# Optimization experiments

Measured on AMD Instinct MI355X. Metric: run time of the kernel, lower is better.

Reference implementation:

```python
import jax, jax.numpy as jnp
import numpy as np

B, C, H, W = 16, 32, 32, 2048


def setup_inputs() -> dict:
    key = jax.random.key(0)
    ks = jax.random.split(key, 7)
    s = 1.0 / np.sqrt(C * H)  # torch conv2d default init scale (fan_in = C*H*1)
    x = jax.random.normal(ks[0], (B, C, H, W), dtype=jnp.float32)
    wq = jax.random.uniform(ks[1], (C, C, H), jnp.float32, -s, s)
    bq = jax.random.uniform(ks[2], (C,), jnp.float32, -s, s)
    wk = jax.random.uniform(ks[3], (C, C, H), jnp.float32, -s, s)
    bk = jax.random.uniform(ks[4], (C,), jnp.float32, -s, s)
    wv = jax.random.uniform(ks[5], (C, C, H), jnp.float32, -s, s)
    bv = jax.random.uniform(ks[6], (C,), jnp.float32, -s, s)
    return {"x": x, "wq": wq, "bq": bq, "wk": wk, "bk": bk, "wv": wv, "bv": bv}


def _proj(x, w, b):
    # Conv2d kernel (H,1) with no padding == contract over (in_channels, H).
    # x: [B,C,H,W], w: [Cout,Cin,H] -> [B,Cout,W]
    return jnp.einsum('bihw,oih->bow', x, w) + b[None, :, None]


def reference(x, wq, bq, wk, bk, wv, bv):
    q = _proj(x, wq, bq)            # [B,C,W]
    k = _proj(x, wk, bk)            # [B,C,W]
    v = _proj(x, wv, bv)            # [B,C,W]
    # query.permute(0,2,1) @ key -> [B,W,W]; NOTE: unscaled, as in source.
    scores = jnp.einsum('bcw,bcv->bwv', q, k)
    attn = jax.nn.softmax(scores, axis=-1)
    # value @ attention^T -> [B,C,W]
    out = jnp.einsum('bcv,bwv->bcw', v, attn)
    # bilinear upsample (1,W)->(H,W), align_corners=False: width is identity,
    # height replicates the single row -> pure broadcast. Then residual add.
    return out[:, :, None, :] + x
```

## Files before the change

kernel.cpp:

```cpp
#include <hip/hip_runtime.h>
#include <hip/hip_bf16.h>

typedef __bf16 bf16x8 __attribute__((ext_vector_type(8)));
typedef float  f32x4  __attribute__((ext_vector_type(4)));
typedef float  f32x16 __attribute__((ext_vector_type(16)));

#define NB 16
#define NC 32
#define NH 32
#define NW 2048
#define NK (NC*NH)

static __device__ __forceinline__ unsigned int pk2(float a, float b) {
    union { __bf16 h[2]; unsigned int u; } z;
    z.h[0] = (__bf16)a; z.h[1] = (__bf16)b;
    return z.u;
}

__global__ __launch_bounds__(256) void wprep_kernel(
    const float* __restrict__ wq, const float* __restrict__ wk,
    const float* __restrict__ wv, __bf16* __restrict__ wb)
{
    const int i = blockIdx.x * 256 + threadIdx.x;
    const float* srcs[3] = { wq, wk, wv };
    const float4 v = *(const float4*)(srcs[i >> 13] + (size_t)(i & 8191) * 4);
    union { __bf16 h[4]; unsigned long long u; } z;
    z.h[0] = (__bf16)v.x; z.h[1] = (__bf16)v.y;
    z.h[2] = (__bf16)v.z; z.h[3] = (__bf16)v.w;
    *(unsigned long long*)(wb + (size_t)i * 4) = z.u;
}

__global__ __launch_bounds__(256, 4) void proj_kernel(
    const float* __restrict__ x, const __bf16* __restrict__ wb,
    const float* __restrict__ bq, const float* __restrict__ bk,
    const float* __restrict__ bv,
    __bf16* __restrict__ qT, __bf16* __restrict__ kT, __bf16* __restrict__ V)
{
    const int b    = blockIdx.x >> 6;
    const int wt   = blockIdx.x & 63;
    const int wave = threadIdx.x >> 6;
    const int lane = threadIdx.x & 63;
    const int g    = lane >> 4;
    const int lr   = lane & 15;
    const int w0   = wt * 32;

    const float* xb = x + (size_t)b * NK * NW;
    const int k0 = wave * 256;

    f32x4 acc[2][6];
    #pragma unroll
    for (int mt = 0; mt < 2; ++mt)
        #pragma unroll
        for (int nt = 0; nt < 6; ++nt)
            acc[mt][nt] = f32x4{0.f, 0.f, 0.f, 0.f};

    for (int ki = 0; ki < 8; ++ki) {
        const int kk = k0 + ki * 32;
        bf16x8 af[2];
        #pragma unroll
        for (int mt = 0; mt < 2; ++mt) {
            const float* p = xb + (size_t)(kk + g*8) * NW + (w0 + mt*16 + lr);
            bf16x8 t;
            #pragma unroll
            for (int j = 0; j < 8; ++j) t[j] = (__bf16)p[(size_t)j * NW];
            af[mt] = t;
        }
        bf16x8 bfv[6];
        #pragma unroll
        for (int nt = 0; nt < 6; ++nt)
            bfv[nt] = *(const bf16x8*)(wb + (size_t)(nt >> 1) * 32768
                                          + (size_t)((nt & 1) * 16 + lr) * NK
                                          + kk + g*8);
        #pragma unroll
        for (int mt = 0; mt < 2; ++mt)
            #pragma unroll
            for (int nt = 0; nt < 6; ++nt)
                acc[mt][nt] = __builtin_amdgcn_mfma_f32_16x16x32_bf16(
                    af[mt], bfv[nt], acc[mt][nt], 0, 0, 0);
    }

    __shared__ f32x4 part[4][6][64];
    const float* biases[3] = { bq, bk, bv };
    #pragma unroll
    for (int mt = 0; mt < 2; ++mt) {
        if (mt) __syncthreads();
        #pragma unroll
        for (int nt = 0; nt < 6; ++nt)
            part[wave][nt][lane] = acc[mt][nt];
        __syncthreads();
        #pragma unroll
        for (int q = 0; q < 2; ++q) {
            const int nt = wave + q * 4;
            if (nt < 6) {
                f32x4 s = part[0][nt][lane];
                #pragma unroll
                for (int sl = 1; sl < 4; ++sl) s += part[sl][nt][lane];
                const int pid = nt >> 1;
                const int o   = (nt & 1) * 16 + lr;
                const float bb = biases[pid][o];
                if (pid < 2) {
                    __bf16* dst = (pid ? kT : qT) + (size_t)b * NW * NC;
                    #pragma unroll
                    for (int r = 0; r < 4; ++r) {
                        const int w = w0 + mt*16 + g*4 + r;
                        dst[(size_t)w * NC + o] = (__bf16)(s[r] + bb);
                    }
                } else {
                    union { __bf16 h[4]; unsigned long long u; } z;
                    #pragma unroll
                    for (int r = 0; r < 4; ++r) z.h[r] = (__bf16)(s[r] + bb);
                    __bf16* dst = V + ((size_t)b * NC + o) * NW + (w0 + mt*16 + g*4);
                    *(unsigned long long*)dst = z.u;
                }
            }
        }
    }
}

__global__ __launch_bounds__(512) void attn_kernel(
    const float* __restrict__ x,
    const __bf16* __restrict__ qT, const __bf16* __restrict__ kT,
    const __bf16* __restrict__ V,
    float* __restrict__ out)
{
    const int b    = blockIdx.x >> 6;
    const int wt   = blockIdx.x & 63;
    const int w0   = wt * 32;
    const int wave = threadIdx.x >> 6;
    const int lane = threadIdx.x & 63;
    const int wl = lane & 31, hi = lane >> 5;
    const int swl = (wl & 0x13) | ((wl & 4) << 1) | ((wl & 8) >> 1);

    const __bf16* qTb = qT + (size_t)b * NW * NC;
    const __bf16* kTb = kT + (size_t)b * NW * NC;
    const __bf16* Vb  = V  + (size_t)b * NC * NW;

    const __bf16* qrow = qTb + (size_t)(w0 + wl) * NC;
    const bf16x8 qf0 = *(const bf16x8*)(qrow + hi*8);
    const bf16x8 qf1 = *(const bf16x8*)(qrow + 16 + hi*8);

    f32x16 acc, z16;
    #pragma unroll
    for (int r = 0; r < 16; ++r) { acc[r] = 0.f; z16[r] = 0.f; }
    float m = -1e30f, lsum = 0.f;

    const int vbeg = wave * 256;
    for (int it = 0; it < 8; ++it) {
        const int v0 = vbeg + it * 32;
        const __bf16* krow = kTb + (size_t)(v0 + swl) * NC;
        const bf16x8 kf0 = *(const bf16x8*)(krow + hi*8);
        const bf16x8 kf1 = *(const bf16x8*)(krow + 16 + hi*8);
        const __bf16* vrow = Vb + (size_t)wl * NW + v0;
        const bf16x8 vf0 = *(const bf16x8*)(vrow + hi*8);
        const bf16x8 vf1 = *(const bf16x8*)(vrow + 16 + hi*8);

        f32x16 s = __builtin_amdgcn_mfma_f32_32x32x16_bf16(kf0, qf0, z16, 0, 0, 0);
        s = __builtin_amdgcn_mfma_f32_32x32x16_bf16(kf1, qf1, s, 0, 0, 0);

        float tm[8];
        #pragma unroll
        for (int r = 0; r < 8; ++r) tm[r] = fmaxf(s[r], s[r+8]);
        #pragma unroll
        for (int r = 0; r < 4; ++r) tm[r] = fmaxf(tm[r], tm[r+4]);
        float vm = fmaxf(fmaxf(tm[0], tm[1]), fmaxf(tm[2], tm[3]));
        vm = fmaxf(vm, __shfl_xor(vm, 32));
        const float nm = fmaxf(m, vm);
        const float sc = __expf(m - nm);
        float p[16];
        #pragma unroll
        for (int r = 0; r < 16; ++r) p[r] = __expf(s[r] - nm);
        float ts[8];
        #pragma unroll
        for (int r = 0; r < 8; ++r) ts[r] = p[r] + p[r+8];
        #pragma unroll
        for (int r = 0; r < 4; ++r) ts[r] += ts[r+4];
        float ps = (ts[0] + ts[1]) + (ts[2] + ts[3]);
        ps += __shfl_xor(ps, 32);
        lsum = lsum * sc + ps;
        m = nm;
        #pragma unroll
        for (int r = 0; r < 16; ++r) acc[r] *= sc;

        union { unsigned int u[4]; bf16x8 v; } pf1, pf2;
        #pragma unroll
        for (int i = 0; i < 4; ++i) pf1.u[i] = pk2(p[2*i],     p[2*i + 1]);
        #pragma unroll
        for (int i = 0; i < 4; ++i) pf2.u[i] = pk2(p[8 + 2*i], p[8 + 2*i + 1]);

        acc = __builtin_amdgcn_mfma_f32_32x32x16_bf16(vf0, pf1.v, acc, 0, 0, 0);
        acc = __builtin_amdgcn_mfma_f32_32x32x16_bf16(vf1, pf2.v, acc, 0, 0, 0);
    }

    __shared__ float sm[8][32];
    __shared__ float sl[8][32];
    __shared__ float sO[8][32][33];
    __shared__ float Of[32][33];

    if (hi == 0) { sm[wave][wl] = m; sl[wave][wl] = lsum; }
    #pragma unroll
    for (int r = 0; r < 16; ++r) {
        const int c = (r & 3) + 8*(r >> 2) + 4*hi;
        sO[wave][c][wl] = acc[r];
    }
    __syncthreads();

    {
        const int w  = threadIdx.x & 31;
        const int c0 = (threadIdx.x >> 5) * 2;
        float ms[8], ls[8], f[8];
        #pragma unroll
        for (int s = 0; s < 8; ++s) { ms[s] = sm[s][w]; ls[s] = sl[s][w]; }
        float M = ms[0];
        #pragma unroll
        for (int s = 1; s < 8; ++s) M = fmaxf(M, ms[s]);
        float L = 0.f;
        #pragma unroll
        for (int s = 0; s < 8; ++s) { f[s] = __expf(ms[s] - M); L += ls[s] * f[s]; }
        const float rL = 1.0f / L;
        #pragma unroll
        for (int cc = 0; cc < 2; ++cc) {
            float o = 0.f;
            #pragma unroll
            for (int s = 0; s < 8; ++s) o += sO[s][c0 + cc][w] * f[s];
            Of[c0 + cc][w] = o * rL;
        }
    }
    __syncthreads();

    const float* xb = x   + (size_t)b * NC * NH * NW + w0;
    float*       ob = out + (size_t)b * NC * NH * NW + w0;
    const int chunk = threadIdx.x & 7;
    #pragma unroll
    for (int it = 0; it < 16; ++it) {
        const int row = it*64 + (threadIdx.x >> 3);
        const int c = row >> 5, h = row & 31;
        const size_t off = ((size_t)c * NH + h) * NW + chunk*4;
        const float4 xv = *(const float4*)(xb + off);
        float4 ov;
        ov.x = Of[c][chunk*4 + 0] + xv.x;
        ov.y = Of[c][chunk*4 + 1] + xv.y;
        ov.z = Of[c][chunk*4 + 2] + xv.z;
        ov.w = Of[c][chunk*4 + 3] + xv.w;
        *(float4*)(ob + off) = ov;
    }
}

extern "C" void kernel_launch(void* const* d_in, const int* in_sizes, int n_in,
                              void* d_out, int out_size, void* d_ws, size_t ws_size,
                              hipStream_t stream)
{
    const float* x  = (const float*)d_in[0];
    const float* wq = (const float*)d_in[1];
    const float* bq = (const float*)d_in[2];
    const float* wk = (const float*)d_in[3];
    const float* bk = (const float*)d_in[4];
    const float* wv = (const float*)d_in[5];
    const float* bv = (const float*)d_in[6];
    float* out = (float*)d_out;

    char* ws = (char*)d_ws;
    __bf16* qT = (__bf16*)(ws);
    __bf16* kT = (__bf16*)(ws + (2u << 20));
    __bf16* V  = (__bf16*)(ws + (4u << 20));
    __bf16* wb = (__bf16*)(ws + (6u << 20));

    hipLaunchKernelGGL(wprep_kernel, dim3(96), dim3(256), 0, stream, wq, wk, wv, wb);
    hipLaunchKernelGGL(proj_kernel, dim3(NB * 64), dim3(256), 0, stream,
                       x, wb, bq, bk, bv, qT, kT, V);
    hipLaunchKernelGGL(attn_kernel, dim3(NB * 64), dim3(512), 0, stream,
                       x, qT, kT, V, out);
}
```

Baseline: 106.7 us.

## Software-pipeline x loads in proj kernel with float2 loads and interleaved columns

The projection kernel now loads x as float2, so each lane covers two adjacent columns that feed the two M tiles, and the M-tile to column mapping is interleaved. The K loop is fully unrolled and double-buffered so the next k-slice's loads are issued before the current slice's MFMAs. The occupancy hint in launch_bounds is removed to allow more registers for the extra buffers. In exchange, the V store becomes four scalar bf16 writes instead of one packed 8-byte write, and register pressure rises.

After: 102.9 us. 3.6% less time.

```diff
diff --git a/kernel.cpp b/kernel.cpp
--- a/kernel.cpp
+++ b/kernel.cpp
@@ -30,7 +30,7 @@
     *(unsigned long long*)(wb + (size_t)i * 4) = z.u;
 }
 
-__global__ __launch_bounds__(256, 4) void proj_kernel(
+__global__ __launch_bounds__(256) void proj_kernel(
     const float* __restrict__ x, const __bf16* __restrict__ wb,
     const float* __restrict__ bq, const float* __restrict__ bk,
     const float* __restrict__ bv,
@@ -46,6 +46,7 @@
 
     const float* xb = x + (size_t)b * NK * NW;
     const int k0 = wave * 256;
+    const float* xcol = xb + (w0 + 2*lr);
 
     f32x4 acc[2][6];
     #pragma unroll
@@ -54,30 +55,46 @@
         for (int nt = 0; nt < 6; ++nt)
             acc[mt][nt] = f32x4{0.f, 0.f, 0.f, 0.f};
 
-    for (int ki = 0; ki < 8; ++ki) {
-        const int kk = k0 + ki * 32;
-        bf16x8 af[2];
-        #pragma unroll
-        for (int mt = 0; mt < 2; ++mt) {
-            const float* p = xb + (size_t)(kk + g*8) * NW + (w0 + mt*16 + lr);
-            bf16x8 t;
-            #pragma unroll
-            for (int j = 0; j < 8; ++j) t[j] = (__bf16)p[(size_t)j * NW];
-            af[mt] = t;
-        }
-        bf16x8 bfv[6];
-        #pragma unroll
-        for (int nt = 0; nt < 6; ++nt)
-            bfv[nt] = *(const bf16x8*)(wb + (size_t)(nt >> 1) * 32768
-                                          + (size_t)((nt & 1) * 16 + lr) * NK
-                                          + kk + g*8);
-        #pragma unroll
-        for (int mt = 0; mt < 2; ++mt)
-            #pragma unroll
-            for (int nt = 0; nt < 6; ++nt)
-                acc[mt][nt] = __builtin_amdgcn_mfma_f32_16x16x32_bf16(
-                    af[mt], bfv[nt], acc[mt][nt], 0, 0, 0);
-    }
+    float2 A0[8], A1[8];
+
+#define LOADA(DST, KK)                                                        \
+    _Pragma("unroll")                                                         \
+    for (int j = 0; j < 8; ++j)                                               \
+        DST[j] = *(const float2*)(xcol + (size_t)((KK) + g*8 + j) * NW);
+
+#define COMPUTE(SRC, KK)                                                      \
+    {                                                                         \
+        bf16x8 af0, af1;                                                      \
+        _Pragma("unroll")                                                     \
+        for (int j = 0; j < 8; ++j) { af0[j] = (__bf16)SRC[j].x;              \
+                                      af1[j] = (__bf16)SRC[j].y; }            \
+        bf16x8 bfv[6];                                                        \
+        _Pragma("unroll")                                                     \
+        for (int nt = 0; nt < 6; ++nt)                                        \
+            bfv[nt] = *(const bf16x8*)(wb + (size_t)(nt >> 1) * 32768         \
+                                          + (size_t)((nt & 1) * 16 + lr) * NK \
+                                          + (KK) + g*8);                      \
+        _Pragma("unroll")                                                     \
+        for (int nt = 0; nt < 6; ++nt) {                                      \
+            acc[0][nt] = __builtin_amdgcn_mfma_f32_16x16x32_bf16(             \
+                af0, bfv[nt], acc[0][nt], 0, 0, 0);                           \
+            acc[1][nt] = __builtin_amdgcn_mfma_f32_16x16x32_bf16(             \
+                af1, bfv[nt], acc[1][nt], 0, 0, 0);                           \
+        }                                                                     \
+    }
+
+    LOADA(A0, k0);
+    #pragma unroll
+    for (int kp = 0; kp < 4; ++kp) {
+        const int kk0 = k0 + (2*kp)     * 32;
+        const int kk1 = k0 + (2*kp + 1) * 32;
+        LOADA(A1, kk1);
+        COMPUTE(A0, kk0);
+        if (kp < 3) { LOADA(A0, kk1 + 32); }
+        COMPUTE(A1, kk1);
+    }
+#undef LOADA
+#undef COMPUTE
 
     __shared__ f32x4 part[4][6][64];
     const float* biases[3] = { bq, bk, bv };
@@ -102,15 +119,16 @@
                     __bf16* dst = (pid ? kT : qT) + (size_t)b * NW * NC;
                     #pragma unroll
                     for (int r = 0; r < 4; ++r) {
-                        const int w = w0 + mt*16 + g*4 + r;
+                        const int w = w0 + 2*(g*4 + r) + mt;
                         dst[(size_t)w * NC + o] = (__bf16)(s[r] + bb);
                     }
                 } else {
-                    union { __bf16 h[4]; unsigned long long u; } z;
+                    __bf16* dst = V + ((size_t)b * NC + o) * NW;
                     #pragma unroll
-                    for (int r = 0; r < 4; ++r) z.h[r] = (__bf16)(s[r] + bb);
-                    __bf16* dst = V + ((size_t)b * NC + o) * NW + (w0 + mt*16 + g*4);
-                    *(unsigned long long*)dst = z.u;
+                    for (int r = 0; r < 4; ++r) {
+                        const int w = w0 + 2*(g*4 + r) + mt;
+                        dst[w] = (__bf16)(s[r] + bb);
+                    }
                 }
             }
         }
```
